# Optimization experiments

Hardware: AMD Instinct MI355X
Metric: run time of the kernel (lower is better)

Reference implementation:

```python
import jax, jax.numpy as jnp
import numpy as np

B, T, D = 32, 2048, 256   # batch, encoder time steps, input_dim
H = 256                   # output_dim (GRU hidden)
A = 128                   # attention_dim
C = 4367                  # nb_classes
STEPS = 22                # max_out_t_steps


def setup_inputs() -> dict:
    key = jax.random.key(0)
    ks = jax.random.split(key, 11)
    s = 0.05
    return {
        "x": jax.random.normal(ks[0], (B, T, D), dtype=jnp.float32),
        # additive attention params: softmax_T(tanh(x Wx + h Wh) @ v)
        "Wx": jax.random.normal(ks[1], (D, A), dtype=jnp.float32) * s,
        "Wh": jax.random.normal(ks[2], (H, A), dtype=jnp.float32) * s,
        "v": jax.random.normal(ks[3], (A,), dtype=jnp.float32) * s,
        # torch GRUCell params
        "W_ih": jax.random.normal(ks[4], (3 * H, D), dtype=jnp.float32) * s,
        "W_hh": jax.random.normal(ks[5], (3 * H, H), dtype=jnp.float32) * s,
        "b_ih": jax.random.normal(ks[6], (3 * H,), dtype=jnp.float32) * s,
        "b_hh": jax.random.normal(ks[7], (3 * H,), dtype=jnp.float32) * s,
        # classifier
        "W_cls": jax.random.normal(ks[8], (C, H), dtype=jnp.float32) * s,
        "b_cls": jax.random.normal(ks[9], (C,), dtype=jnp.float32) * s,
    }


def reference(x, Wx, Wh, v, W_ih, W_hh, b_ih, b_hh, W_cls, b_cls):
    # dropout layers are identity in eval/reference mode
    xW = jnp.einsum("btd,da->bta", x, Wx)  # hoisted: constant across steps
    h0 = jnp.zeros((x.shape[0], H), dtype=x.dtype)

    def step(h, _):
        # additive attention over time axis
        e = jnp.einsum("bta,a->bt", jnp.tanh(xW + (h @ Wh)[:, None, :]), v)
        att = jax.nn.softmax(e, axis=1)          # [B, T]
        ctx = jnp.einsum("btd,bt->bd", x, att)   # weighted sum over T
        # torch GRUCell
        gi = ctx @ W_ih.T + b_ih                  # [B, 3H]
        gh = h @ W_hh.T + b_hh                    # [B, 3H]
        i_r, i_z, i_n = jnp.split(gi, 3, axis=1)
        h_r, h_z, h_n = jnp.split(gh, 3, axis=1)
        r = jax.nn.sigmoid(i_r + h_r)
        z = jax.nn.sigmoid(i_z + h_z)
        n = jnp.tanh(i_n + r * h_n)
        h_new = (1.0 - z) * n + z * h
        logits = h_new @ W_cls.T + b_cls          # [B, C]
        return h_new, logits

    _, outs = jax.lax.scan(step, h0, None, length=STEPS)  # [STEPS, B, C]
    return jnp.transpose(outs, (1, 0, 2))                 # [B, STEPS, C]
```

## Files before the change

### kernel.cpp

```cpp
#include <hip/hip_runtime.h>

#define BB 32
#define TT 2048
#define DD 256
#define HH 256
#define AA 128
#define CC 4367
#define CLS_LD 4480
#define NSTEPS 22
#define NCHUNK 32

typedef unsigned short ushortT;
typedef unsigned int uintT;
typedef unsigned long long u64T;
using frag8 = __attribute__((ext_vector_type(8))) short;
using f32x4 = __attribute__((ext_vector_type(4))) float;

__device__ __forceinline__ float tanh_fast(float u) {
  float e = __expf(2.0f * u);
  return 1.0f - 2.0f / (e + 1.0f);
}
__device__ __forceinline__ float sigmoid_fast(float u) {
  return 1.0f / (1.0f + __expf(-u));
}
__device__ __forceinline__ ushortT f2bf(float f) {
  unsigned int u = __float_as_uint(f);
  unsigned int r = (u + 0x7FFFu + ((u >> 16) & 1u)) >> 16;
  return (ushortT)r;
}
__device__ __forceinline__ float bf2f(ushortT v) {
  return __uint_as_float(((unsigned int)v) << 16);
}

__global__ __launch_bounds__(256) void trans_kernel(
    const float* __restrict__ Wx, const float* __restrict__ W_cls,
    float* __restrict__ WclsT, ushortT* __restrict__ WxT_bf) {
  int blk = blockIdx.x;
  __shared__ float tile[32][33];
  const int li = threadIdx.x >> 5, lj = threadIdx.x & 31;
  if (blk < 1096) {
    int i0 = (blk >> 3) * 32, j0 = (blk & 7) * 32;
#pragma unroll
    for (int k = 0; k < 4; ++k) {
      int i = i0 + li + k * 8;
      if (i < CC) tile[li + k * 8][lj] = W_cls[(size_t)i * 256 + j0 + lj];
    }
    __syncthreads();
#pragma unroll
    for (int k = 0; k < 4; ++k) {
      int j = j0 + li + k * 8, i = i0 + lj;
      if (i < CC) WclsT[(size_t)j * CLS_LD + i] = tile[lj][li + k * 8];
    }
  } else {
    blk -= 1096;
    int i0 = (blk >> 2) * 32, j0 = (blk & 3) * 32;
#pragma unroll
    for (int k = 0; k < 4; ++k)
      tile[li + k * 8][lj] = Wx[(size_t)(i0 + li + k * 8) * 128 + j0 + lj];
    __syncthreads();
#pragma unroll
    for (int k = 0; k < 4; ++k) {
      int j = j0 + li + k * 8;
      WxT_bf[(size_t)j * 256 + i0 + lj] = f2bf(tile[lj][li + k * 8]);
    }
  }
}

__global__ __launch_bounds__(256) void xw_mfma(
    const float* __restrict__ x, const ushortT* __restrict__ WxT_bf,
    ushortT* __restrict__ x_bf, ushortT* __restrict__ xW_ta) {
  __shared__ ushortT lds[2 * 128 * 72];
#define SX(r, c) lds[(r) * 72 + (c)]
#define SW(r, c) lds[128 * 72 + (r) * 72 + (c)]
#define ST(m, a) lds[(m) * 136 + (a)]
  const int tid = threadIdx.x;
  const int lane = tid & 63, w = tid >> 6;
  const int l15 = lane & 15, quad = lane >> 4;
  const int r0 = blockIdx.x * 128;
  const int row = tid >> 1, half = tid & 1;

  f32x4 acc[2][8];
#pragma unroll
  for (int mt = 0; mt < 2; ++mt)
#pragma unroll
    for (int nt = 0; nt < 8; ++nt) acc[mt][nt] = (f32x4){0.f, 0.f, 0.f, 0.f};

  for (int kk0 = 0; kk0 < 256; kk0 += 64) {
    {
      const float4* xp = (const float4*)(x + (size_t)(r0 + row) * DD + kk0 + half * 32);
      uint4 pk[4];
#pragma unroll
      for (int i = 0; i < 4; ++i) {
        float4 f0 = xp[2 * i], f1 = xp[2 * i + 1];
        pk[i].x = (uintT)f2bf(f0.x) | ((uintT)f2bf(f0.y) << 16);
        pk[i].y = (uintT)f2bf(f0.z) | ((uintT)f2bf(f0.w) << 16);
        pk[i].z = (uintT)f2bf(f1.x) | ((uintT)f2bf(f1.y) << 16);
        pk[i].w = (uintT)f2bf(f1.z) | ((uintT)f2bf(f1.w) << 16);
      }
      uint4* sxp = (uint4*)&SX(row, half * 32);
      uint4* gxp = (uint4*)(x_bf + (size_t)(r0 + row) * DD + kk0 + half * 32);
#pragma unroll
      for (int i = 0; i < 4; ++i) { sxp[i] = pk[i]; gxp[i] = pk[i]; }
    }
    {
      const uint4* wp = (const uint4*)(WxT_bf + (size_t)row * DD + kk0 + half * 32);
      uint4* swp = (uint4*)&SW(row, half * 32);
#pragma unroll
      for (int i = 0; i < 4; ++i) swp[i] = wp[i];
    }
    __syncthreads();
#pragma unroll
    for (int kk = 0; kk < 2; ++kk) {
      frag8 a0 = *(const frag8*)&SX(w * 32 + l15, kk * 32 + quad * 8);
      frag8 a1 = *(const frag8*)&SX(w * 32 + 16 + l15, kk * 32 + quad * 8);
#pragma unroll
      for (int nt = 0; nt < 8; ++nt) {
        frag8 bf = *(const frag8*)&SW(nt * 16 + l15, kk * 32 + quad * 8);
        acc[0][nt] = __builtin_amdgcn_mfma_f32_16x16x32_bf16(a0, bf, acc[0][nt], 0, 0, 0);
        acc[1][nt] = __builtin_amdgcn_mfma_f32_16x16x32_bf16(a1, bf, acc[1][nt], 0, 0, 0);
      }
    }
    __syncthreads();
  }
#pragma unroll
  for (int mt = 0; mt < 2; ++mt)
#pragma unroll
    for (int nt = 0; nt < 8; ++nt)
#pragma unroll
      for (int r = 0; r < 4; ++r) {
        int m = w * 32 + mt * 16 + quad * 4 + r;
        int a = nt * 16 + l15;
        ST(m, a) = f2bf(acc[mt][nt][r]);
      }
  __syncthreads();
  {
    const uint4* sp = (const uint4*)&ST(row, half * 64);
    uint4* gp = (uint4*)(xW_ta + (size_t)(r0 + row) * AA + half * 64);
#pragma unroll
    for (int i = 0; i < 8; ++i) gp[i] = sp[i];
  }
#undef SX
#undef SW
#undef ST
}

__global__ __launch_bounds__(256) void gates_kernel(
    const float* __restrict__ ctx_part, const float* __restrict__ den_part,
    const float* __restrict__ hall_c, const float* __restrict__ W_ih,
    const float* __restrict__ W_hh, const float* __restrict__ b_ih,
    const float* __restrict__ b_hh, const float* __restrict__ Wh,
    float* __restrict__ hall, float* __restrict__ hWh_part, int s) {
  const int sl = blockIdx.x, b = blockIdx.y, tid = threadIdx.x;
  __shared__ __align__(16) float sctx[DD];
  __shared__ float sden;
  __shared__ float sh16[16];
  if (tid < 32) {
    float d = den_part[b * NCHUNK + tid];
#pragma unroll
    for (int off = 16; off > 0; off >>= 1) d += __shfl_down(d, off, 32);
    if (tid == 0) sden = d;
  }
  {
    float acc = 0.f;
#pragma unroll
    for (int c = 0; c < NCHUNK; ++c)
      acc += ctx_part[((size_t)b * NCHUNK + c) * DD + tid];
    sctx[tid] = acc;
  }
  __syncthreads();
  const float invd = 1.0f / sden;
  const int kq = tid & 15, gsub = tid >> 4;
  const float4* cp = (const float4*)sctx + kq * 4;
  const float4* hrow = (s >= 2) ? (const float4*)(hall_c + ((size_t)(s - 2) * BB + b) * HH) + kq * 4 : nullptr;
  float4 c4[4], h4[4];
#pragma unroll
  for (int j = 0; j < 4; ++j) {
    float4 cv = cp[j];
    c4[j].x = cv.x * invd; c4[j].y = cv.y * invd; c4[j].z = cv.z * invd; c4[j].w = cv.w * invd;
    if (hrow) h4[j] = hrow[j];
    else { h4[j].x = 0.f; h4[j].y = 0.f; h4[j].z = 0.f; h4[j].w = 0.f; }
  }
  float gi_g[3], gh_g[3];
#pragma unroll
  for (int it = 0; it < 3; ++it) {
    const int g = it * 256 + sl * 16 + gsub;
    const float4* wi = (const float4*)(W_ih + (size_t)g * DD) + kq * 4;
    const float4* wh = (const float4*)(W_hh + (size_t)g * HH) + kq * 4;
    float gi = 0.f, gh = 0.f;
#pragma unroll
    for (int j = 0; j < 4; ++j) {
      float4 wv = wi[j];
      gi += c4[j].x * wv.x + c4[j].y * wv.y + c4[j].z * wv.z + c4[j].w * wv.w;
      wv = wh[j];
      gh += h4[j].x * wv.x + h4[j].y * wv.y + h4[j].z * wv.z + h4[j].w * wv.w;
    }
#pragma unroll
    for (int off = 8; off > 0; off >>= 1) {
      gi += __shfl_down(gi, off, 16);
      gh += __shfl_down(gh, off, 16);
    }
    gi_g[it] = gi + b_ih[g];
    gh_g[it] = gh + b_hh[g];
  }
  if (kq == 0) {
    const int i = sl * 16 + gsub;
    float hp = (s >= 2) ? hall_c[((size_t)(s - 2) * BB + b) * HH + i] : 0.f;
    float r = sigmoid_fast(gi_g[0] + gh_g[0]);
    float z = sigmoid_fast(gi_g[1] + gh_g[1]);
    float n = tanh_fast(gi_g[2] + r * gh_g[2]);
    float hv = (1.f - z) * n + z * hp;
    hall[((size_t)(s - 1) * BB + b) * HH + i] = hv;
    sh16[gsub] = hv;
  }
  __syncthreads();
  if (tid < AA) {
    float acc = 0.f;
#pragma unroll
    for (int k = 0; k < 16; ++k)
      acc = fmaf(sh16[k], Wh[(size_t)(sl * 16 + k) * AA + tid], acc);
    hWh_part[((size_t)b * 16 + sl) * AA + tid] = acc;
  }
}

__global__ __launch_bounds__(256, 4) void att_kernel(
    const ushortT* __restrict__ x_bf, const ushortT* __restrict__ xW_ta,
    const float* __restrict__ hWh_part, const float* __restrict__ v,
    float* __restrict__ ctx_part, float* __restrict__ den_part) {
  const int tid = threadIdx.x;
  const int b = blockIdx.x;
  const int chunk = blockIdx.y;
  const int t0 = chunk * 64;
  __shared__ float sh_hWh[AA], sh_v[AA];
  __shared__ float sh_w[64];
  __shared__ __align__(16) float sh_ctx[4 * DD];
  if (tid < AA) {
    float hw = 0.f;
    if (hWh_part) {
#pragma unroll
      for (int sl = 0; sl < 16; ++sl)
        hw += hWh_part[((size_t)b * 16 + sl) * AA + tid];
    }
    sh_hWh[tid] = hw;
    sh_v[tid] = v[tid];
  }
  __syncthreads();
  const int j4 = tid >> 6, dq = tid & 63;
  u64T xr[16];
  {
    const u64T* xb4 = (const u64T*)x_bf;
#pragma unroll
    for (int j = 0; j < 16; ++j)
      xr[j] = xb4[(((size_t)(b * TT + t0 + j * 4 + j4)) * DD >> 2) + dq];
  }
  {
    const int tl = tid >> 2, aseg = tid & 3;
    const uint4* xw16 = (const uint4*)(xW_ta + (size_t)(b * TT + t0 + tl) * AA + aseg * 32);
    float e = 0.f;
#pragma unroll
    for (int i = 0; i < 4; ++i) {
      uint4 u = xw16[i];
      const int ab = aseg * 32 + i * 8;
      e = fmaf(tanh_fast(bf2f((ushortT)(u.x & 0xFFFFu)) + sh_hWh[ab + 0]), sh_v[ab + 0], e);
      e = fmaf(tanh_fast(bf2f((ushortT)(u.x >> 16)) + sh_hWh[ab + 1]), sh_v[ab + 1], e);
      e = fmaf(tanh_fast(bf2f((ushortT)(u.y & 0xFFFFu)) + sh_hWh[ab + 2]), sh_v[ab + 2], e);
      e = fmaf(tanh_fast(bf2f((ushortT)(u.y >> 16)) + sh_hWh[ab + 3]), sh_v[ab + 3], e);
      e = fmaf(tanh_fast(bf2f((ushortT)(u.z & 0xFFFFu)) + sh_hWh[ab + 4]), sh_v[ab + 4], e);
      e = fmaf(tanh_fast(bf2f((ushortT)(u.z >> 16)) + sh_hWh[ab + 5]), sh_v[ab + 5], e);
      e = fmaf(tanh_fast(bf2f((ushortT)(u.w & 0xFFFFu)) + sh_hWh[ab + 6]), sh_v[ab + 6], e);
      e = fmaf(tanh_fast(bf2f((ushortT)(u.w >> 16)) + sh_hWh[ab + 7]), sh_v[ab + 7], e);
    }
    e += __shfl_xor(e, 1, 4);
    e += __shfl_xor(e, 2, 4);
    if (aseg == 0) sh_w[tl] = __expf(e);
  }
  __syncthreads();
  {
    float4 acc = {0.f, 0.f, 0.f, 0.f};
#pragma unroll
    for (int j = 0; j < 16; ++j) {
      float w = sh_w[j * 4 + j4];
      u64T u = xr[j];
      acc.x = fmaf(w, bf2f((ushortT)(u       & 0xFFFFu)), acc.x);
      acc.y = fmaf(w, bf2f((ushortT)((u >> 16) & 0xFFFFu)), acc.y);
      acc.z = fmaf(w, bf2f((ushortT)((u >> 32) & 0xFFFFu)), acc.z);
      acc.w = fmaf(w, bf2f((ushortT)((u >> 48) & 0xFFFFu)), acc.w);
    }
    ((float4*)sh_ctx)[j4 * 64 + dq] = acc;
  }
  __syncthreads();
  {
    float sum = sh_ctx[tid] + sh_ctx[DD + tid] + sh_ctx[2 * DD + tid] + sh_ctx[3 * DD + tid];
    ctx_part[((size_t)b * NCHUNK + chunk) * DD + tid] = sum;
  }
  if (tid < 64) {
    float ds = sh_w[tid];
#pragma unroll
    for (int off = 32; off > 0; off >>= 1) ds += __shfl_down(ds, off, 64);
    if (tid == 0) den_part[b * NCHUNK + chunk] = ds;
  }
}

__global__ __launch_bounds__(256) void cls_kernel(
    const float* __restrict__ hall, const float* __restrict__ WclsT,
    const float* __restrict__ b_cls, float* __restrict__ out) {
  const int tid = threadIdx.x;
  const int c0 = blockIdx.x * 128;
  const int r0 = blockIdx.y * 32;
  const int cq = tid & 31, rg = tid >> 5;
  const int c = c0 + cq * 4;
  __shared__ __align__(16) float shh[32 * HH];
  {
    const float4* hsrc = (const float4*)(hall + (size_t)r0 * HH);
    float4* hdst = (float4*)shh;
#pragma unroll
    for (int i = 0; i < 8; ++i) hdst[tid + 256 * i] = hsrc[tid + 256 * i];
  }
  __syncthreads();
  float acc[4][4];
#pragma unroll
  for (int j = 0; j < 4; ++j)
#pragma unroll
    for (int l = 0; l < 4; ++l) acc[j][l] = 0.f;
#pragma unroll 4
  for (int k = 0; k < HH; ++k) {
    float4 w4 = *(const float4*)(WclsT + (size_t)k * CLS_LD + c);
    float h0 = shh[(rg * 4 + 0) * HH + k];
    float h1 = shh[(rg * 4 + 1) * HH + k];
    float h2 = shh[(rg * 4 + 2) * HH + k];
    float h3 = shh[(rg * 4 + 3) * HH + k];
    acc[0][0] = fmaf(h0, w4.x, acc[0][0]); acc[0][1] = fmaf(h0, w4.y, acc[0][1]);
    acc[0][2] = fmaf(h0, w4.z, acc[0][2]); acc[0][3] = fmaf(h0, w4.w, acc[0][3]);
    acc[1][0] = fmaf(h1, w4.x, acc[1][0]); acc[1][1] = fmaf(h1, w4.y, acc[1][1]);
    acc[1][2] = fmaf(h1, w4.z, acc[1][2]); acc[1][3] = fmaf(h1, w4.w, acc[1][3]);
    acc[2][0] = fmaf(h2, w4.x, acc[2][0]); acc[2][1] = fmaf(h2, w4.y, acc[2][1]);
    acc[2][2] = fmaf(h2, w4.z, acc[2][2]); acc[2][3] = fmaf(h2, w4.w, acc[2][3]);
    acc[3][0] = fmaf(h3, w4.x, acc[3][0]); acc[3][1] = fmaf(h3, w4.y, acc[3][1]);
    acc[3][2] = fmaf(h3, w4.z, acc[3][2]); acc[3][3] = fmaf(h3, w4.w, acc[3][3]);
  }
#pragma unroll
  for (int j = 0; j < 4; ++j) {
    int row = r0 + rg * 4 + j;
    int bb = row & (BB - 1), st = row >> 5;
    size_t obase = ((size_t)bb * NSTEPS + st) * CC;
#pragma unroll
    for (int l = 0; l < 4; ++l) {
      int cc = c + l;
      if (cc < CC) out[obase + cc] = acc[j][l] + b_cls[cc];
    }
  }
}

extern "C" void kernel_launch(void* const* d_in, const int* in_sizes, int n_in,
                              void* d_out, int out_size, void* d_ws, size_t ws_size,
                              hipStream_t stream) {
  const float* x     = (const float*)d_in[0];
  const float* Wx    = (const float*)d_in[1];
  const float* Wh    = (const float*)d_in[2];
  const float* v     = (const float*)d_in[3];
  const float* W_ih  = (const float*)d_in[4];
  const float* W_hh  = (const float*)d_in[5];
  const float* b_ih  = (const float*)d_in[6];
  const float* b_hh  = (const float*)d_in[7];
  const float* W_cls = (const float*)d_in[8];
  const float* b_cls = (const float*)d_in[9];
  float* out = (float*)d_out;

  float* ctx_part = (float*)d_ws;
  float* den_part = ctx_part + (size_t)BB * NCHUNK * DD;
  float* hWh_part = den_part + BB * NCHUNK;
  float* hall     = hWh_part + (size_t)BB * 16 * AA;
  float* WclsT    = hall + (size_t)NSTEPS * BB * HH;
  ushortT* WxT_bf = (ushortT*)(WclsT + (size_t)256 * CLS_LD);
  ushortT* x_bf   = WxT_bf + 128 * 256;
  ushortT* xW_ta  = x_bf + (size_t)BB * TT * DD;

  trans_kernel<<<1096 + 32, 256, 0, stream>>>(Wx, W_cls, WclsT, WxT_bf);
  xw_mfma<<<(BB * TT) / 128, 256, 0, stream>>>(x, WxT_bf, x_bf, xW_ta);

  att_kernel<<<dim3(BB, NCHUNK), 256, 0, stream>>>(x_bf, xW_ta, nullptr, v, ctx_part, den_part);
  for (int s = 1; s <= NSTEPS; ++s) {
    gates_kernel<<<dim3(16, BB), 256, 0, stream>>>(ctx_part, den_part, hall, W_ih, W_hh,
                                                   b_ih, b_hh, Wh, hall, hWh_part, s);
    if (s < NSTEPS)
      att_kernel<<<dim3(BB, NCHUNK), 256, 0, stream>>>(x_bf, xW_ta, hWh_part, v, ctx_part, den_part);
  }
  cls_kernel<<<dim3(35, 22), 256, 0, stream>>>(hall, WclsT, b_cls, out);
}
```

Measured before the change: 596.0 us.

## Process two batch rows per gates block and prefetch next K-tile in xw_mfma

The GRU gates kernel now handles two batch rows per block, so each W_ih/W_hh weight fetch is reused for two dot products and the grid halves. The xW MFMA kernel loads the next 64-wide K slice of x and Wx into registers while the current slice is being multiplied, overlapping global loads with compute. This raises register pressure in both kernels. The gates change mainly cuts weight traffic in a small kernel that is launched 22 times.

New measurement: 597.1 us. About the same (+0.2%).

```diff
diff --git a/kernel.cpp b/kernel.cpp
--- a/kernel.cpp
+++ b/kernel.cpp
@@ -85,13 +85,23 @@
 #pragma unroll
     for (int nt = 0; nt < 8; ++nt) acc[mt][nt] = (f32x4){0.f, 0.f, 0.f, 0.f};
 
-  for (int kk0 = 0; kk0 < 256; kk0 += 64) {
+  float4 xraw[8];
+  uint4 wraw[4];
+  {
+    const float4* xp = (const float4*)(x + (size_t)(r0 + row) * DD + half * 32);
+    const uint4* wp = (const uint4*)(WxT_bf + (size_t)row * DD + half * 32);
+#pragma unroll
+    for (int i = 0; i < 8; ++i) xraw[i] = xp[i];
+#pragma unroll
+    for (int i = 0; i < 4; ++i) wraw[i] = wp[i];
+  }
+  for (int it = 0; it < 4; ++it) {
+    const int kk0 = it * 64;
     {
-      const float4* xp = (const float4*)(x + (size_t)(r0 + row) * DD + kk0 + half * 32);
       uint4 pk[4];
 #pragma unroll
       for (int i = 0; i < 4; ++i) {
-        float4 f0 = xp[2 * i], f1 = xp[2 * i + 1];
+        float4 f0 = xraw[2 * i], f1 = xraw[2 * i + 1];
         pk[i].x = (uintT)f2bf(f0.x) | ((uintT)f2bf(f0.y) << 16);
         pk[i].y = (uintT)f2bf(f0.z) | ((uintT)f2bf(f0.w) << 16);
         pk[i].z = (uintT)f2bf(f1.x) | ((uintT)f2bf(f1.y) << 16);
@@ -99,16 +109,22 @@
       }
       uint4* sxp = (uint4*)&SX(row, half * 32);
       uint4* gxp = (uint4*)(x_bf + (size_t)(r0 + row) * DD + kk0 + half * 32);
+      uint4* swp = (uint4*)&SW(row, half * 32);
 #pragma unroll
       for (int i = 0; i < 4; ++i) { sxp[i] = pk[i]; gxp[i] = pk[i]; }
-    }
-    {
-      const uint4* wp = (const uint4*)(WxT_bf + (size_t)row * DD + kk0 + half * 32);
-      uint4* swp = (uint4*)&SW(row, half * 32);
-#pragma unroll
-      for (int i = 0; i < 4; ++i) swp[i] = wp[i];
+#pragma unroll
+      for (int i = 0; i < 4; ++i) swp[i] = wraw[i];
     }
     __syncthreads();
+    if (it < 3) {
+      const int kn = kk0 + 64;
+      const float4* xp = (const float4*)(x + (size_t)(r0 + row) * DD + kn + half * 32);
+      const uint4* wp = (const uint4*)(WxT_bf + (size_t)row * DD + kn + half * 32);
+#pragma unroll
+      for (int i = 0; i < 8; ++i) xraw[i] = xp[i];
+#pragma unroll
+      for (int i = 0; i < 4; ++i) wraw[i] = wp[i];
+    }
 #pragma unroll
     for (int kk = 0; kk < 2; ++kk) {
       frag8 a0 = *(const frag8*)&SX(w * 32 + l15, kk * 32 + quad * 8);
@@ -150,75 +166,98 @@
     const float* __restrict__ W_hh, const float* __restrict__ b_ih,
     const float* __restrict__ b_hh, const float* __restrict__ Wh,
     float* __restrict__ hall, float* __restrict__ hWh_part, int s) {
-  const int sl = blockIdx.x, b = blockIdx.y, tid = threadIdx.x;
-  __shared__ __align__(16) float sctx[DD];
-  __shared__ float sden;
-  __shared__ float sh16[16];
-  if (tid < 32) {
-    float d = den_part[b * NCHUNK + tid];
+  const int sl = blockIdx.x, bp = blockIdx.y, tid = threadIdx.x;
+  const int b0 = bp * 2;
+  __shared__ __align__(16) float sctx[2][DD];
+  __shared__ float sden[2];
+  __shared__ float sh16[2][16];
+  if (tid < 64) {
+    const int bb = tid >> 5, l = tid & 31;
+    float d = den_part[(b0 + bb) * NCHUNK + l];
 #pragma unroll
     for (int off = 16; off > 0; off >>= 1) d += __shfl_down(d, off, 32);
-    if (tid == 0) sden = d;
-  }
-  {
+    if (l == 0) sden[bb] = d;
+  }
+#pragma unroll
+  for (int bb = 0; bb < 2; ++bb) {
     float acc = 0.f;
 #pragma unroll
     for (int c = 0; c < NCHUNK; ++c)
-      acc += ctx_part[((size_t)b * NCHUNK + c) * DD + tid];
-    sctx[tid] = acc;
-  }
-  __syncthreads();
-  const float invd = 1.0f / sden;
+      acc += ctx_part[((size_t)(b0 + bb) * NCHUNK + c) * DD + tid];
+    sctx[bb][tid] = acc;
+  }
+  __syncthreads();
+  const float invd0 = 1.0f / sden[0], invd1 = 1.0f / sden[1];
   const int kq = tid & 15, gsub = tid >> 4;
-  const float4* cp = (const float4*)sctx + kq * 4;
-  const float4* hrow = (s >= 2) ? (const float4*)(hall_c + ((size_t)(s - 2) * BB + b) * HH) + kq * 4 : nullptr;
-  float4 c4[4], h4[4];
+  float4 c4[2][4], h4[2][4];
 #pragma unroll
   for (int j = 0; j < 4; ++j) {
-    float4 cv = cp[j];
-    c4[j].x = cv.x * invd; c4[j].y = cv.y * invd; c4[j].z = cv.z * invd; c4[j].w = cv.w * invd;
-    if (hrow) h4[j] = hrow[j];
-    else { h4[j].x = 0.f; h4[j].y = 0.f; h4[j].z = 0.f; h4[j].w = 0.f; }
-  }
-  float gi_g[3], gh_g[3];
+    float4 cv = ((const float4*)sctx[0])[kq * 4 + j];
+    c4[0][j].x = cv.x * invd0; c4[0][j].y = cv.y * invd0;
+    c4[0][j].z = cv.z * invd0; c4[0][j].w = cv.w * invd0;
+    cv = ((const float4*)sctx[1])[kq * 4 + j];
+    c4[1][j].x = cv.x * invd1; c4[1][j].y = cv.y * invd1;
+    c4[1][j].z = cv.z * invd1; c4[1][j].w = cv.w * invd1;
+    h4[0][j].x = 0.f; h4[0][j].y = 0.f; h4[0][j].z = 0.f; h4[0][j].w = 0.f;
+    h4[1][j] = h4[0][j];
+  }
+  if (s >= 2) {
+#pragma unroll
+    for (int bb = 0; bb < 2; ++bb) {
+      const float4* hp = (const float4*)(hall_c + ((size_t)(s - 2) * BB + b0 + bb) * HH) + kq * 4;
+#pragma unroll
+      for (int j = 0; j < 4; ++j) h4[bb][j] = hp[j];
+    }
+  }
+  float gi_g[2][3], gh_g[2][3];
 #pragma unroll
   for (int it = 0; it < 3; ++it) {
     const int g = it * 256 + sl * 16 + gsub;
     const float4* wi = (const float4*)(W_ih + (size_t)g * DD) + kq * 4;
     const float4* wh = (const float4*)(W_hh + (size_t)g * HH) + kq * 4;
-    float gi = 0.f, gh = 0.f;
+    float gi0 = 0.f, gi1 = 0.f, gh0 = 0.f, gh1 = 0.f;
 #pragma unroll
     for (int j = 0; j < 4; ++j) {
       float4 wv = wi[j];
-      gi += c4[j].x * wv.x + c4[j].y * wv.y + c4[j].z * wv.z + c4[j].w * wv.w;
+      gi0 += c4[0][j].x * wv.x + c4[0][j].y * wv.y + c4[0][j].z * wv.z + c4[0][j].w * wv.w;
+      gi1 += c4[1][j].x * wv.x + c4[1][j].y * wv.y + c4[1][j].z * wv.z + c4[1][j].w * wv.w;
       wv = wh[j];
-      gh += h4[j].x * wv.x + h4[j].y * wv.y + h4[j].z * wv.z + h4[j].w * wv.w;
+      gh0 += h4[0][j].x * wv.x + h4[0][j].y * wv.y + h4[0][j].z * wv.z + h4[0][j].w * wv.w;
+      gh1 += h4[1][j].x * wv.x + h4[1][j].y * wv.y + h4[1][j].z * wv.z + h4[1][j].w * wv.w;
     }
 #pragma unroll
     for (int off = 8; off > 0; off >>= 1) {
-      gi += __shfl_down(gi, off, 16);
-      gh += __shfl_down(gh, off, 16);
-    }
-    gi_g[it] = gi + b_ih[g];
-    gh_g[it] = gh + b_hh[g];
+      gi0 += __shfl_down(gi0, off, 16);
+      gi1 += __shfl_down(gi1, off, 16);
+      gh0 += __shfl_down(gh0, off, 16);
+      gh1 += __shfl_down(gh1, off, 16);
+    }
+    gi_g[0][it] = gi0 + b_ih[g];
+    gi_g[1][it] = gi1 + b_ih[g];
+    gh_g[0][it] = gh0 + b_hh[g];
+    gh_g[1][it] = gh1 + b_hh[g];
   }
   if (kq == 0) {
     const int i = sl * 16 + gsub;
-    float hp = (s >= 2) ? hall_c[((size_t)(s - 2) * BB + b) * HH + i] : 0.f;
-    float r = sigmoid_fast(gi_g[0] + gh_g[0]);
-    float z = sigmoid_fast(gi_g[1] + gh_g[1]);
-    float n = tanh_fast(gi_g[2] + r * gh_g[2]);
-    float hv = (1.f - z) * n + z * hp;
-    hall[((size_t)(s - 1) * BB + b) * HH + i] = hv;
-    sh16[gsub] = hv;
-  }
-  __syncthreads();
-  if (tid < AA) {
+#pragma unroll
+    for (int bb = 0; bb < 2; ++bb) {
+      float hp = (s >= 2) ? hall_c[((size_t)(s - 2) * BB + b0 + bb) * HH + i] : 0.f;
+      float r = sigmoid_fast(gi_g[bb][0] + gh_g[bb][0]);
+      float z = sigmoid_fast(gi_g[bb][1] + gh_g[bb][1]);
+      float n = tanh_fast(gi_g[bb][2] + r * gh_g[bb][2]);
+      float hv = (1.f - z) * n + z * hp;
+      hall[((size_t)(s - 1) * BB + b0 + bb) * HH + i] = hv;
+      sh16[bb][gsub] = hv;
+    }
+  }
+  __syncthreads();
+  {
+    const int bb = tid >> 7, a = tid & 127;
     float acc = 0.f;
 #pragma unroll
     for (int k = 0; k < 16; ++k)
-      acc = fmaf(sh16[k], Wh[(size_t)(sl * 16 + k) * AA + tid], acc);
-    hWh_part[((size_t)b * 16 + sl) * AA + tid] = acc;
+      acc = fmaf(sh16[bb][k], Wh[(size_t)(sl * 16 + k) * AA + a], acc);
+    hWh_part[((size_t)(b0 + bb) * 16 + sl) * AA + a] = acc;
   }
 }
 
@@ -379,7 +418,7 @@
 
   att_kernel<<<dim3(BB, NCHUNK), 256, 0, stream>>>(x_bf, xW_ta, nullptr, v, ctx_part, den_part);
   for (int s = 1; s <= NSTEPS; ++s) {
-    gates_kernel<<<dim3(16, BB), 256, 0, stream>>>(ctx_part, den_part, hall, W_ih, W_hh,
+    gates_kernel<<<dim3(16, 16), 256, 0, stream>>>(ctx_part, den_part, hall, W_ih, W_hh,
                                                    b_ih, b_hh, Wh, hall, hWh_part, s);
     if (s < NSTEPS)
       att_kernel<<<dim3(BB, NCHUNK), 256, 0, stream>>>(x_bf, xW_ta, hWh_part, v, ctx_part, den_part);
```
